# Performance work log

Measured on AMD Instinct MI355X. Metric: run time of the kernel, lower is better.

The kernel has to match this reference:

```python
import jax, jax.numpy as jnp
import numpy as np

B, S = 128, 32
V, E, H, L = 32000, 512, 1024, 2


def setup_inputs() -> dict:
    key = jax.random.key(0)
    ks = jax.random.split(key, 16)
    s = 0.02  # weight scale
    inp = {
        "x": jax.random.randint(ks[0], (B, S), 0, V),
        "encoder_output": jax.random.normal(ks[1], (S, B, H), jnp.float32),  # unused by module
        "encoder_hidden_state": jax.random.normal(ks[2], (L, B, H), jnp.float32),
        "emb": jax.random.normal(ks[3], (V, E), jnp.float32) * s,
        "w_ih0": jax.random.normal(ks[4], (3 * H, E), jnp.float32) * s,
        "w_hh0": jax.random.normal(ks[5], (3 * H, H), jnp.float32) * s,
        "b_ih0": jax.random.normal(ks[6], (3 * H,), jnp.float32) * s,
        "b_hh0": jax.random.normal(ks[7], (3 * H,), jnp.float32) * s,
        "w_ih1": jax.random.normal(ks[8], (3 * H, H), jnp.float32) * s,
        "w_hh1": jax.random.normal(ks[9], (3 * H, H), jnp.float32) * s,
        "b_ih1": jax.random.normal(ks[10], (3 * H,), jnp.float32) * s,
        "b_hh1": jax.random.normal(ks[11], (3 * H,), jnp.float32) * s,
        "w_dec": jax.random.normal(ks[12], (V, H), jnp.float32) * s,
        "b_dec": jax.random.normal(ks[13], (V,), jnp.float32) * s,
        "max_seq_length": S,
    }
    return inp


def _gru_cell(h, xt, w_ih, w_hh, b_ih, b_hh):
    # PyTorch GRU gate math
    gi = xt @ w_ih.T + b_ih  # [B, 3H]
    gh = h @ w_hh.T + b_hh   # [B, 3H]
    ir, iz, inn = jnp.split(gi, 3, axis=-1)
    hr, hz, hn = jnp.split(gh, 3, axis=-1)
    r = jax.nn.sigmoid(ir + hr)
    z = jax.nn.sigmoid(iz + hz)
    n = jnp.tanh(inn + r * hn)
    return (1.0 - z) * n + z * h


def reference(x, encoder_output, encoder_hidden_state, emb,
              w_ih0, w_hh0, b_ih0, b_hh0,
              w_ih1, w_hh1, b_ih1, b_hh1,
              w_dec, b_dec, max_seq_length):
    # teaching_rate = 0.0 -> pure teacher forcing; dropout p=0.0 -> identity.
    # Step 0 consumes SOS token (id 1, from torch.ones().long()); steps 1..T-1 consume x[:, i].
    Bsz = x.shape[0]
    sos = jnp.ones((Bsz, 1), jnp.int32)
    toks = jnp.concatenate([sos, x[:, 1:max_seq_length].astype(jnp.int32)], axis=1)  # [B, T]
    xs = emb[toks].transpose(1, 0, 2)  # [T, B, E] (seq-first, matching permute(1,0,2))

    def step(carry, xt):
        h0, h1 = carry
        h0 = _gru_cell(h0, xt, w_ih0, w_hh0, b_ih0, b_hh0)
        h1 = _gru_cell(h1, h0, w_ih1, w_hh1, b_ih1, b_hh1)
        return (h0, h1), h1

    init = (encoder_hidden_state[0], encoder_hidden_state[1])
    _, ys = jax.lax.scan(step, init, xs)  # ys: [T, B, H]
    logits = jnp.einsum('tbh,vh->tbv', ys, w_dec) + b_dec  # [T, B, V]
    return logits
```

## Files before the change

kernel.cpp:

```cpp
#include <hip/hip_runtime.h>
#include <hip/hip_bf16.h>
#include <stdint.h>

#define T_SEQ 32
#define BATCH 128
#define EMB   512
#define HID   1024
#define VOC   32000
#define G3    (3 * HID)
#define MROWS (T_SEQ * BATCH)
#define BHID  (BATCH * HID)

typedef __bf16 bf16_t;
typedef __bf16 bf16x8 __attribute__((ext_vector_type(8)));
typedef __bf16 bf16x4 __attribute__((ext_vector_type(4)));
typedef float  f32x4  __attribute__((ext_vector_type(4)));

#define MFMA(a, b, c) __builtin_amdgcn_mfma_f32_16x16x32_bf16((a), (b), (c), 0, 0, 0)

__global__ void f32_to_bf16_kernel(const float* __restrict__ in,
                                   bf16_t* __restrict__ out, int n) {
    int i = (blockIdx.x * blockDim.x + threadIdx.x) * 4;
    if (i + 3 < n) {
        float4 v = *(const float4*)(in + i);
        out[i + 0] = (bf16_t)v.x;
        out[i + 1] = (bf16_t)v.y;
        out[i + 2] = (bf16_t)v.z;
        out[i + 3] = (bf16_t)v.w;
    } else {
        for (; i < n; ++i) out[i] = (bf16_t)in[i];
    }
}

__global__ void embed_kernel(const int* __restrict__ x,
                             const float* __restrict__ emb,
                             bf16_t* __restrict__ X) {
    int m = blockIdx.x;
    int t = m >> 7, b = m & 127;
    int tok = (t == 0) ? 1 : x[b * T_SEQ + t];
    const float* src = emb + (size_t)tok * EMB;
    bf16_t* dst = X + (size_t)m * EMB;
    int c = threadIdx.x * 4;
    float4 v = *(const float4*)(src + c);
    dst[c + 0] = (bf16_t)v.x;
    dst[c + 1] = (bf16_t)v.y;
    dst[c + 2] = (bf16_t)v.z;
    dst[c + 3] = (bf16_t)v.w;
}

#define GLOAD_LDS16(g, l)                                                    \
    __builtin_amdgcn_global_load_lds(                                        \
        (const __attribute__((address_space(1))) void*)(g),                  \
        (__attribute__((address_space(3))) void*)(l), 16, 0, 0)

template <int BIAS>
__global__ __launch_bounds__(256) void gemm_bf16_kernel(
    const bf16_t* __restrict__ A, const bf16_t* __restrict__ B,
    const float* __restrict__ bias, float* __restrict__ C,
    int M, int N, int K) {
    __shared__ __align__(16) bf16_t As[128 * 32];
    __shared__ __align__(16) bf16_t Bs[128 * 32];

    const int nbm = gridDim.y, nbn = gridDim.x;
    const int nwg = nbm * nbn;
    int lin = blockIdx.y * nbn + blockIdx.x;
    if ((nwg & 7) == 0) {
        int xcd = lin & 7, idx = lin >> 3;
        lin = xcd * (nwg >> 3) + idx;
    }
    const int bm = (lin % nbm) * 128;
    const int bn = (lin / nbm) * 128;

    const int tid  = threadIdx.x;
    const int lane = tid & 63;
    const int w    = tid >> 6;
    const int wr   = w >> 1, wc = w & 1;

    f32x4 acc[4][4] = {};

    const int lrow = tid >> 2;
    const int lcol = (tid & 3) * 8;
    const bf16_t* ag = A + (size_t)(bm + lrow) * K + lcol;
    const bf16_t* bg = B + (size_t)(bn + lrow) * K + lcol;
    bf16_t* asl0 = As + lrow * 32 + lcol;
    bf16_t* asl1 = As + (lrow + 64) * 32 + lcol;
    bf16_t* bsl0 = Bs + lrow * 32 + lcol;
    bf16_t* bsl1 = Bs + (lrow + 64) * 32 + lcol;

    const int r16 = lane & 15;
    const int kh  = (lane >> 4) * 8;

    for (int k0 = 0; k0 < K; k0 += 32) {
        GLOAD_LDS16(ag + k0, asl0);
        GLOAD_LDS16(ag + (size_t)64 * K + k0, asl1);
        GLOAD_LDS16(bg + k0, bsl0);
        GLOAD_LDS16(bg + (size_t)64 * K + k0, bsl1);
        __syncthreads();

        bf16x8 af[4], bf[4];
#pragma unroll
        for (int mi = 0; mi < 4; ++mi)
            af[mi] = *(const bf16x8*)(As + (wr * 64 + mi * 16 + r16) * 32 + kh);
#pragma unroll
        for (int ni = 0; ni < 4; ++ni)
            bf[ni] = *(const bf16x8*)(Bs + (wc * 64 + ni * 16 + r16) * 32 + kh);
#pragma unroll
        for (int mi = 0; mi < 4; ++mi)
#pragma unroll
            for (int ni = 0; ni < 4; ++ni)
                acc[mi][ni] = MFMA(af[mi], bf[ni], acc[mi][ni]);
        __syncthreads();
    }

#pragma unroll
    for (int mi = 0; mi < 4; ++mi) {
        const int row0 = bm + wr * 64 + mi * 16 + (lane >> 4) * 4;
#pragma unroll
        for (int ni = 0; ni < 4; ++ni) {
            const int col = bn + wc * 64 + ni * 16 + r16;
            float bv = 0.f;
            if (BIAS) bv = bias[col];
#pragma unroll
            for (int r = 0; r < 4; ++r)
                C[(size_t)(row0 + r) * N + col] = acc[mi][ni][r] + bv;
        }
    }
}

template <int BIAS>
__global__ __launch_bounds__(512, 1) void gemm256_bf16_kernel(
    const bf16_t* __restrict__ A, const bf16_t* __restrict__ B,
    const float* __restrict__ bias, float* __restrict__ C,
    int M, int N, int K) {
    __shared__ __align__(16) bf16_t lds[2 * 2 * 16384];

    const int NT = K >> 6;
    const int nbm = gridDim.y, nbn = gridDim.x;
    const int nwg = nbm * nbn;
    int lin = blockIdx.y * nbn + blockIdx.x;
    {
        int q = nwg >> 3, r = nwg & 7, x = lin & 7, i = lin >> 3;
        lin = (x < r ? x * (q + 1) : r * (q + 1) + (x - r) * q) + i;
    }
    const int bm = (lin % nbm) * 256;
    const int bn = (lin / nbm) * 256;

    const int tid = threadIdx.x, lane = tid & 63;
    const int w = tid >> 6, wm = w >> 2, wn = w & 3;
    const int r16 = lane & 15, sl = lane >> 4, r7 = r16 & 7;

    const int srow  = tid >> 3;
    const int sslot = (tid & 7) ^ (srow & 7);
    const bf16_t* agS = A + (size_t)(bm + srow) * K + sslot * 8;
    const bf16_t* bgS = B + (size_t)(bn + srow) * K + sslot * 8;

    const int colk0 = ((0 + sl) ^ r7) * 8;
    const int colk1 = ((4 + sl) ^ r7) * 8;
    const int arow = (wm * 128 + r16) * 64;
    const int brow = (wn * 64 + r16) * 64;

    f32x4 acc[8][4] = {};
    bf16x8 af[4][2], bf[4][2];

#pragma unroll
    for (int l = 0; l < 4; ++l)
        GLOAD_LDS16(agS + (size_t)(l * 64) * K, lds + l * 4096 + tid * 8);
#pragma unroll
    for (int l = 0; l < 4; ++l)
        GLOAD_LDS16(bgS + (size_t)(l * 64) * K, lds + 16384 + l * 4096 + tid * 8);
#pragma unroll
    for (int l = 0; l < 4; ++l)
        GLOAD_LDS16(agS + (size_t)(l * 64) * K + 64,
                    lds + 32768 + l * 4096 + tid * 8);
#pragma unroll
    for (int l = 0; l < 4; ++l)
        GLOAD_LDS16(bgS + (size_t)(l * 64) * K + 64,
                    lds + 49152 + l * 4096 + tid * 8);
    asm volatile("s_waitcnt vmcnt(8)" ::: "memory");
    __builtin_amdgcn_sched_barrier(0);
    __builtin_amdgcn_s_barrier();

#pragma unroll 1
    for (int kt = 0; kt < NT; ++kt) {
        const int cur = kt & 1;
        const bf16_t* Ab = lds + cur * 32768;
        const bf16_t* Bb = Ab + 16384;
        bf16_t* Sb = lds + cur * 32768;
        const bool st = (kt + 2 < NT);
        const size_t kof = (size_t)(kt + 2) * 64;

#pragma unroll
        for (int fr = 0; fr < 4; ++fr) {
            af[fr][0] = *(const bf16x8*)(Ab + arow + fr * 1024 + colk0);
            af[fr][1] = *(const bf16x8*)(Ab + arow + fr * 1024 + colk1);
        }
#pragma unroll
        for (int nf = 0; nf < 2; ++nf) {
            bf[nf][0] = *(const bf16x8*)(Bb + brow + nf * 1024 + colk0);
            bf[nf][1] = *(const bf16x8*)(Bb + brow + nf * 1024 + colk1);
        }
        __builtin_amdgcn_sched_barrier(0);
        __builtin_amdgcn_s_barrier();
        asm volatile("s_waitcnt lgkmcnt(0)" ::: "memory");
        __builtin_amdgcn_sched_barrier(0);
        __builtin_amdgcn_s_setprio(1);
#pragma unroll
        for (int fr = 0; fr < 4; ++fr)
#pragma unroll
            for (int nf = 0; nf < 2; ++nf) {
                acc[fr][nf] = MFMA(af[fr][0], bf[nf][0], acc[fr][nf]);
                acc[fr][nf] = MFMA(af[fr][1], bf[nf][1], acc[fr][nf]);
            }
        __builtin_amdgcn_s_setprio(0);
        __builtin_amdgcn_sched_barrier(0);
        __builtin_amdgcn_s_barrier();

#pragma unroll
        for (int nf = 2; nf < 4; ++nf) {
            bf[nf][0] = *(const bf16x8*)(Bb + brow + nf * 1024 + colk0);
            bf[nf][1] = *(const bf16x8*)(Bb + brow + nf * 1024 + colk1);
        }
        __builtin_amdgcn_sched_barrier(0);
        if (st) {
            GLOAD_LDS16(agS + kof, Sb + tid * 8);
            GLOAD_LDS16(agS + (size_t)128 * K + kof, Sb + 8192 + tid * 8);
        }
        __builtin_amdgcn_s_barrier();
        asm volatile("s_waitcnt lgkmcnt(0)" ::: "memory");
        __builtin_amdgcn_sched_barrier(0);
        __builtin_amdgcn_s_setprio(1);
#pragma unroll
        for (int fr = 0; fr < 4; ++fr)
#pragma unroll
            for (int nf = 2; nf < 4; ++nf) {
                acc[fr][nf] = MFMA(af[fr][0], bf[nf][0], acc[fr][nf]);
                acc[fr][nf] = MFMA(af[fr][1], bf[nf][1], acc[fr][nf]);
            }
        __builtin_amdgcn_s_setprio(0);
        __builtin_amdgcn_sched_barrier(0);
        __builtin_amdgcn_s_barrier();

#pragma unroll
        for (int fr = 0; fr < 4; ++fr) {
            af[fr][0] = *(const bf16x8*)(Ab + arow + (fr + 4) * 1024 + colk0);
            af[fr][1] = *(const bf16x8*)(Ab + arow + (fr + 4) * 1024 + colk1);
        }
        __builtin_amdgcn_sched_barrier(0);
        if (st) {
#pragma unroll
            for (int l = 0; l < 4; ++l)
                GLOAD_LDS16(bgS + (size_t)(l * 64) * K + kof,
                            Sb + 16384 + l * 4096 + tid * 8);
        }
        __builtin_amdgcn_s_barrier();
        asm volatile("s_waitcnt lgkmcnt(0)" ::: "memory");
        __builtin_amdgcn_sched_barrier(0);
        __builtin_amdgcn_s_setprio(1);
#pragma unroll
        for (int fr = 0; fr < 4; ++fr)
#pragma unroll
            for (int nf = 0; nf < 2; ++nf) {
                acc[fr + 4][nf] = MFMA(af[fr][0], bf[nf][0], acc[fr + 4][nf]);
                acc[fr + 4][nf] = MFMA(af[fr][1], bf[nf][1], acc[fr + 4][nf]);
            }
        __builtin_amdgcn_s_setprio(0);
        __builtin_amdgcn_sched_barrier(0);
        __builtin_amdgcn_s_barrier();

        if (st) {
            GLOAD_LDS16(agS + (size_t)64 * K + kof, Sb + 4096 + tid * 8);
            GLOAD_LDS16(agS + (size_t)192 * K + kof, Sb + 12288 + tid * 8);
        }
        if (kt + 2 < NT) {
            asm volatile("s_waitcnt vmcnt(8)" ::: "memory");
        } else if (kt + 1 < NT) {
            asm volatile("s_waitcnt vmcnt(0)" ::: "memory");
        }
        __builtin_amdgcn_sched_barrier(0);
        __builtin_amdgcn_s_setprio(1);
#pragma unroll
        for (int fr = 0; fr < 4; ++fr)
#pragma unroll
            for (int nf = 2; nf < 4; ++nf) {
                acc[fr + 4][nf] = MFMA(af[fr][0], bf[nf][0], acc[fr + 4][nf]);
                acc[fr + 4][nf] = MFMA(af[fr][1], bf[nf][1], acc[fr + 4][nf]);
            }
        __builtin_amdgcn_s_setprio(0);
        __builtin_amdgcn_sched_barrier(0);
        __builtin_amdgcn_s_barrier();
    }

#pragma unroll
    for (int fr = 0; fr < 8; ++fr) {
        const int row0 = bm + wm * 128 + fr * 16 + sl * 4;
#pragma unroll
        for (int nf = 0; nf < 4; ++nf) {
            const int col = bn + wn * 64 + nf * 16 + r16;
            float bv = 0.f;
            if (BIAS) bv = bias[col];
#pragma unroll
            for (int r = 0; r < 4; ++r)
                C[(size_t)(row0 + r) * N + col] = acc[fr][nf][r] + bv;
        }
    }
}

union U64cast  { bf16x4 v; unsigned long long u; };
union U128cast { f32x4 v; unsigned long long u[2]; };

__global__ __launch_bounds__(256, 1) void fused_scan_kernel(
    const bf16_t* __restrict__ h0ib, const bf16_t* __restrict__ h1ib,
    const float* __restrict__ enc_hid,
    const bf16_t* __restrict__ whh0, const bf16_t* __restrict__ wih1,
    const bf16_t* __restrict__ whh1,
    const float* __restrict__ bhh0, const float* __restrict__ bih1,
    const float* __restrict__ bhh1,
    float* __restrict__ Gi, bf16_t* __restrict__ H0b,
    bf16_t* __restrict__ H1b, unsigned* __restrict__ flags) {
    __shared__ __align__(16) float Sg[4][3][128][16];

    const int tid  = threadIdx.x;
    const int lane = tid & 63;
    const int w    = tid >> 6;
    const int role = blockIdx.x >> 6;
    const int cb   = blockIdx.x & 63;
    const int c0   = cb * 16;
    const int r16  = lane & 15;
    const int kq   = (lane >> 4) * 8;

    const bf16_t* whh = role == 0 ? whh0 : (role == 1 ? wih1 : whh1);
    const float*  bia = role == 0 ? bhh0 : (role == 1 ? bih1 : bhh1);

    bf16x8 wf[3][8];
#pragma unroll
    for (int g = 0; g < 3; ++g)
#pragma unroll
        for (int kf = 0; kf < 8; ++kf)
            wf[g][kf] = *(const bf16x8*)(
                whh + (size_t)(g * HID + c0 + r16) * HID + w * 256 + kf * 32 + kq);

    const int cg   = tid & 3;
    const int rloc = tid >> 2;
    const int ce   = c0 + cg * 4;

    float bh[3][4];
#pragma unroll
    for (int g = 0; g < 3; ++g)
#pragma unroll
        for (int j = 0; j < 4; ++j) bh[g][j] = bia[g * HID + ce + j];

    float hp[2][4];
    if (role != 1) {
        const float* h0f = enc_hid + (role == 2 ? BHID : 0);
#pragma unroll
        for (int i = 0; i < 2; ++i)
#pragma unroll
            for (int j = 0; j < 4; ++j)
                hp[i][j] = h0f[(size_t)(rloc + i * 64) * HID + ce + j];
    }

    for (int t = 0; t < T_SEQ; ++t) {
        if (role == 0) {
            if (t && tid < 64)
                while (__hip_atomic_load(&flags[tid], __ATOMIC_RELAXED,
                                         __HIP_MEMORY_SCOPE_SYSTEM) <
                       (unsigned)t)
                    __builtin_amdgcn_s_sleep(1);
        } else if (role == 1) {
            if (tid < 64)
                while (__hip_atomic_load(&flags[tid], __ATOMIC_RELAXED,
                                         __HIP_MEMORY_SCOPE_SYSTEM) <
                       (unsigned)(t + 1))
                    __builtin_amdgcn_s_sleep(1);
        } else {
            if (tid < 64) {
                while (__hip_atomic_load(&flags[64 + tid], __ATOMIC_RELAXED,
                                         __HIP_MEMORY_SCOPE_SYSTEM) <
                       (unsigned)(t + 1))
                    __builtin_amdgcn_s_sleep(1);
            } else if (tid < 128 && t) {
                while (__hip_atomic_load(&flags[128 + tid - 64],
                                         __ATOMIC_RELAXED,
                                         __HIP_MEMORY_SCOPE_SYSTEM) <
                       (unsigned)t)
                    __builtin_amdgcn_s_sleep(1);
            }
        }
        __syncthreads();

        f32x4 gi[2][3];
        if (role == 0) {
#pragma unroll
            for (int i = 0; i < 2; ++i) {
                const size_t gb =
                    ((size_t)t * BATCH + rloc + i * 64) * G3 + ce;
                gi[i][0] = *(const f32x4*)(Gi + gb);
                gi[i][1] = *(const f32x4*)(Gi + gb + HID);
                gi[i][2] = *(const f32x4*)(Gi + gb + 2 * HID);
            }
        } else if (role == 2) {
#pragma unroll
            for (int i = 0; i < 2; ++i) {
                const size_t gb =
                    ((size_t)t * BATCH + rloc + i * 64) * G3 + ce;
#pragma unroll
                for (int g = 0; g < 3; ++g) {
                    U128cast u;
                    const unsigned long long* p =
                        (const unsigned long long*)(Gi + gb + g * HID);
                    u.u[0] = __hip_atomic_load(p, __ATOMIC_RELAXED,
                                               __HIP_MEMORY_SCOPE_SYSTEM);
                    u.u[1] = __hip_atomic_load(p + 1, __ATOMIC_RELAXED,
                                               __HIP_MEMORY_SCOPE_SYSTEM);
                    gi[i][g] = u.v;
                }
            }
        }

        const bf16_t* hb =
            role == 0 ? (t ? H0b + (size_t)(t - 1) * BHID : h0ib)
          : role == 1 ? (H0b + (size_t)t * BHID)
                      : (t ? H1b + (size_t)(t - 1) * BHID : h1ib);

        f32x4 acc[3][8] = {};
        bf16x8 af[4][8];
#define LD_GROUP(buf, kf)                                                    \
    {                                                                        \
        const int kbase = w * 256 + (kf) * 32 + kq;                          \
        _Pragma("unroll") for (int rf = 0; rf < 8; ++rf)                     \
            af[buf][rf] =                                                    \
                *(const bf16x8*)(hb + (size_t)(rf * 16 + r16) * HID + kbase); \
    }
        LD_GROUP(0, 0)
        LD_GROUP(1, 1)
        LD_GROUP(2, 2)
#pragma unroll
        for (int kf = 0; kf < 8; ++kf) {
            if (kf + 3 < 8) LD_GROUP((kf + 3) & 3, kf + 3)
#pragma unroll
            for (int rf = 0; rf < 8; ++rf) {
                acc[0][rf] = MFMA(af[kf & 3][rf], wf[0][kf], acc[0][rf]);
                acc[1][rf] = MFMA(af[kf & 3][rf], wf[1][kf], acc[1][rf]);
                acc[2][rf] = MFMA(af[kf & 3][rf], wf[2][kf], acc[2][rf]);
            }
        }
#undef LD_GROUP

#pragma unroll
        for (int g = 0; g < 3; ++g)
#pragma unroll
            for (int rf = 0; rf < 8; ++rf)
#pragma unroll
                for (int r = 0; r < 4; ++r)
                    Sg[w][g][rf * 16 + (lane >> 4) * 4 + r][r16] = acc[g][rf][r];
        __syncthreads();

#pragma unroll
        for (int i = 0; i < 2; ++i) {
            const int row = rloc + i * 64;
            f32x4 gr = *(const f32x4*)&Sg[0][0][row][cg * 4];
            f32x4 gz = *(const f32x4*)&Sg[0][1][row][cg * 4];
            f32x4 gn = *(const f32x4*)&Sg[0][2][row][cg * 4];
#pragma unroll
            for (int ks = 1; ks < 4; ++ks) {
                gr += *(const f32x4*)&Sg[ks][0][row][cg * 4];
                gz += *(const f32x4*)&Sg[ks][1][row][cg * 4];
                gn += *(const f32x4*)&Sg[ks][2][row][cg * 4];
            }
            if (role == 1) {
                const size_t gb =
                    ((size_t)t * BATCH + row) * G3 + ce;
                U128cast s0, s1, s2;
#pragma unroll
                for (int j = 0; j < 4; ++j) {
                    s0.v[j] = gr[j] + bh[0][j];
                    s1.v[j] = gz[j] + bh[1][j];
                    s2.v[j] = gn[j] + bh[2][j];
                }
                unsigned long long* p0 = (unsigned long long*)(Gi + gb);
                unsigned long long* p1 = (unsigned long long*)(Gi + gb + HID);
                unsigned long long* p2 = (unsigned long long*)(Gi + gb + 2 * HID);
                __hip_atomic_store(p0, s0.u[0], __ATOMIC_RELAXED, __HIP_MEMORY_SCOPE_SYSTEM);
                __hip_atomic_store(p0 + 1, s0.u[1], __ATOMIC_RELAXED, __HIP_MEMORY_SCOPE_SYSTEM);
                __hip_atomic_store(p1, s1.u[0], __ATOMIC_RELAXED, __HIP_MEMORY_SCOPE_SYSTEM);
                __hip_atomic_store(p1 + 1, s1.u[1], __ATOMIC_RELAXED, __HIP_MEMORY_SCOPE_SYSTEM);
                __hip_atomic_store(p2, s2.u[0], __ATOMIC_RELAXED, __HIP_MEMORY_SCOPE_SYSTEM);
                __hip_atomic_store(p2 + 1, s2.u[1], __ATOMIC_RELAXED, __HIP_MEMORY_SCOPE_SYSTEM);
            } else {
                U64cast hb4;
#pragma unroll
                for (int j = 0; j < 4; ++j) {
                    float rr = 1.f / (1.f + __expf(-(gi[i][0][j] + gr[j] + bh[0][j])));
                    float zz = 1.f / (1.f + __expf(-(gi[i][1][j] + gz[j] + bh[1][j])));
                    float nn = tanhf(gi[i][2][j] + rr * (gn[j] + bh[2][j]));
                    float h  = (1.f - zz) * nn + zz * hp[i][j];
                    hp[i][j] = h;
                    hb4.v[j] = (bf16_t)h;
                }
                bf16_t* dst = (role == 0 ? H0b : H1b) +
                              (size_t)t * BHID + (size_t)row * HID + ce;
                __hip_atomic_store((unsigned long long*)dst, hb4.u,
                                   __ATOMIC_RELAXED, __HIP_MEMORY_SCOPE_SYSTEM);
            }
        }

        __syncthreads();
        if (tid == 0)
            __hip_atomic_store(&flags[role * 64 + cb], (unsigned)(t + 1),
                               __ATOMIC_RELAXED, __HIP_MEMORY_SCOPE_SYSTEM);
    }
}

extern "C" void kernel_launch(void* const* d_in, const int* in_sizes, int n_in,
                              void* d_out, int out_size, void* d_ws, size_t ws_size,
                              hipStream_t stream) {
    const int*   x        = (const int*)d_in[0];
    const float* enc_hid  = (const float*)d_in[2];
    const float* emb      = (const float*)d_in[3];
    const float* w_ih0    = (const float*)d_in[4];
    const float* w_hh0    = (const float*)d_in[5];
    const float* b_ih0    = (const float*)d_in[6];
    const float* b_hh0    = (const float*)d_in[7];
    const float* w_ih1    = (const float*)d_in[8];
    const float* w_hh1    = (const float*)d_in[9];
    const float* b_ih1    = (const float*)d_in[10];
    const float* b_hh1    = (const float*)d_in[11];
    const float* w_dec    = (const float*)d_in[12];
    const float* b_dec    = (const float*)d_in[13];
    float* out = (float*)d_out;

    char* ws = (char*)d_ws;
    size_t off = 0;
    auto alloc = [&](size_t bytes) {
        void* p = ws + off;
        off += (bytes + 255) & ~(size_t)255;
        return p;
    };
    unsigned* flags  = (unsigned*)alloc(1024);
    bf16_t* Xb     = (bf16_t*)alloc((size_t)MROWS * EMB * 2);
    bf16_t* Wih0b  = (bf16_t*)alloc((size_t)G3 * EMB * 2);
    bf16_t* Whh0b  = (bf16_t*)alloc((size_t)G3 * HID * 2);
    bf16_t* Wih1b  = (bf16_t*)alloc((size_t)G3 * HID * 2);
    bf16_t* Whh1b  = (bf16_t*)alloc((size_t)G3 * HID * 2);
    bf16_t* Wdecb  = (bf16_t*)alloc((size_t)VOC * HID * 2);
    bf16_t* h0ib   = (bf16_t*)alloc((size_t)BATCH * HID * 2);
    bf16_t* h1ib   = (bf16_t*)alloc((size_t)BATCH * HID * 2);
    float*  Gi     = (float*)alloc((size_t)MROWS * G3 * 4);
    bf16_t* H0b    = (bf16_t*)alloc((size_t)MROWS * HID * 2);
    bf16_t* H1b    = (bf16_t*)alloc((size_t)MROWS * HID * 2);

    hipMemsetAsync(flags, 0, 1024, stream);

    auto cvt = [&](const float* src, bf16_t* dst, int n) {
        int blocks = (n + 1023) / 1024;
        f32_to_bf16_kernel<<<blocks, 256, 0, stream>>>(src, dst, n);
    };

    cvt(w_ih0, Wih0b, G3 * EMB);
    cvt(w_hh0, Whh0b, G3 * HID);
    cvt(w_ih1, Wih1b, G3 * HID);
    cvt(w_hh1, Whh1b, G3 * HID);
    cvt(w_dec, Wdecb, VOC * HID);
    cvt(enc_hid, h0ib, BATCH * HID);
    cvt(enc_hid + BATCH * HID, h1ib, BATCH * HID);

    embed_kernel<<<MROWS, 128, 0, stream>>>(x, emb, Xb);

    gemm_bf16_kernel<1><<<dim3(G3 / 128, MROWS / 128), 256, 0, stream>>>(
        Xb, Wih0b, b_ih0, Gi, MROWS, G3, EMB);

    fused_scan_kernel<<<192, 256, 0, stream>>>(
        h0ib, h1ib, enc_hid, Whh0b, Wih1b, Whh1b,
        b_hh0, b_ih1, b_hh1, Gi, H0b, H1b, flags);

    gemm256_bf16_kernel<1><<<dim3(VOC / 256, MROWS / 256), 512, 0, stream>>>(
        H1b, Wdecb, b_dec, out, MROWS, VOC, HID);
}
```

Before: 947.0 us.

## Fuse GRU scan and decoder GEMM into persistent mega-kernel with flag-gated tiles

The recurrent scan and the vocabulary projection GEMM now run in one persistent kernel. 192 blocks run the GRU scan while the other 64 blocks pull 256x256 decoder tiles from an atomic counter. Each tile waits only on the layer-1 flags for the timesteps it covers, so the projection can start on early timesteps while later steps are still being computed. This is meant to hide the sequential scan latency behind the large GEMM. The costs are heavier block shapes (512 threads with half idle in scan blocks), co-residency and deadlock risk, and the counter has to be reset between calls.

```diff
diff --git a/kernel.cpp b/kernel.cpp
--- a/kernel.cpp
+++ b/kernel.cpp
@@ -10,6 +10,7 @@
 #define G3    (3 * HID)
 #define MROWS (T_SEQ * BATCH)
 #define BHID  (BATCH * HID)
+#define NTILE 2000
 
 typedef __bf16 bf16_t;
 typedef __bf16 bf16x8 __attribute__((ext_vector_type(8)));
@@ -17,6 +18,16 @@
 typedef float  f32x4  __attribute__((ext_vector_type(4)));
 
 #define MFMA(a, b, c) __builtin_amdgcn_mfma_f32_16x16x32_bf16((a), (b), (c), 0, 0, 0)
+
+union U64cast  { bf16x4 v; unsigned long long u; };
+union U128cast { f32x4 v; unsigned long long u[2]; };
+
+__device__ __forceinline__ unsigned flag_ld(const unsigned* p) {
+    return __hip_atomic_load(p, __ATOMIC_RELAXED, __HIP_MEMORY_SCOPE_SYSTEM);
+}
+__device__ __forceinline__ void flag_st(unsigned* p, unsigned v) {
+    __hip_atomic_store(p, v, __ATOMIC_RELAXED, __HIP_MEMORY_SCOPE_SYSTEM);
+}
 
 __global__ void f32_to_bf16_kernel(const float* __restrict__ in,
                                    bf16_t* __restrict__ out, int n) {
@@ -127,188 +138,7 @@
     }
 }
 
-template <int BIAS>
-__global__ __launch_bounds__(512, 1) void gemm256_bf16_kernel(
-    const bf16_t* __restrict__ A, const bf16_t* __restrict__ B,
-    const float* __restrict__ bias, float* __restrict__ C,
-    int M, int N, int K) {
-    __shared__ __align__(16) bf16_t lds[2 * 2 * 16384];
-
-    const int NT = K >> 6;
-    const int nbm = gridDim.y, nbn = gridDim.x;
-    const int nwg = nbm * nbn;
-    int lin = blockIdx.y * nbn + blockIdx.x;
-    {
-        int q = nwg >> 3, r = nwg & 7, x = lin & 7, i = lin >> 3;
-        lin = (x < r ? x * (q + 1) : r * (q + 1) + (x - r) * q) + i;
-    }
-    const int bm = (lin % nbm) * 256;
-    const int bn = (lin / nbm) * 256;
-
-    const int tid = threadIdx.x, lane = tid & 63;
-    const int w = tid >> 6, wm = w >> 2, wn = w & 3;
-    const int r16 = lane & 15, sl = lane >> 4, r7 = r16 & 7;
-
-    const int srow  = tid >> 3;
-    const int sslot = (tid & 7) ^ (srow & 7);
-    const bf16_t* agS = A + (size_t)(bm + srow) * K + sslot * 8;
-    const bf16_t* bgS = B + (size_t)(bn + srow) * K + sslot * 8;
-
-    const int colk0 = ((0 + sl) ^ r7) * 8;
-    const int colk1 = ((4 + sl) ^ r7) * 8;
-    const int arow = (wm * 128 + r16) * 64;
-    const int brow = (wn * 64 + r16) * 64;
-
-    f32x4 acc[8][4] = {};
-    bf16x8 af[4][2], bf[4][2];
-
-#pragma unroll
-    for (int l = 0; l < 4; ++l)
-        GLOAD_LDS16(agS + (size_t)(l * 64) * K, lds + l * 4096 + tid * 8);
-#pragma unroll
-    for (int l = 0; l < 4; ++l)
-        GLOAD_LDS16(bgS + (size_t)(l * 64) * K, lds + 16384 + l * 4096 + tid * 8);
-#pragma unroll
-    for (int l = 0; l < 4; ++l)
-        GLOAD_LDS16(agS + (size_t)(l * 64) * K + 64,
-                    lds + 32768 + l * 4096 + tid * 8);
-#pragma unroll
-    for (int l = 0; l < 4; ++l)
-        GLOAD_LDS16(bgS + (size_t)(l * 64) * K + 64,
-                    lds + 49152 + l * 4096 + tid * 8);
-    asm volatile("s_waitcnt vmcnt(8)" ::: "memory");
-    __builtin_amdgcn_sched_barrier(0);
-    __builtin_amdgcn_s_barrier();
-
-#pragma unroll 1
-    for (int kt = 0; kt < NT; ++kt) {
-        const int cur = kt & 1;
-        const bf16_t* Ab = lds + cur * 32768;
-        const bf16_t* Bb = Ab + 16384;
-        bf16_t* Sb = lds + cur * 32768;
-        const bool st = (kt + 2 < NT);
-        const size_t kof = (size_t)(kt + 2) * 64;
-
-#pragma unroll
-        for (int fr = 0; fr < 4; ++fr) {
-            af[fr][0] = *(const bf16x8*)(Ab + arow + fr * 1024 + colk0);
-            af[fr][1] = *(const bf16x8*)(Ab + arow + fr * 1024 + colk1);
-        }
-#pragma unroll
-        for (int nf = 0; nf < 2; ++nf) {
-            bf[nf][0] = *(const bf16x8*)(Bb + brow + nf * 1024 + colk0);
-            bf[nf][1] = *(const bf16x8*)(Bb + brow + nf * 1024 + colk1);
-        }
-        __builtin_amdgcn_sched_barrier(0);
-        __builtin_amdgcn_s_barrier();
-        asm volatile("s_waitcnt lgkmcnt(0)" ::: "memory");
-        __builtin_amdgcn_sched_barrier(0);
-        __builtin_amdgcn_s_setprio(1);
-#pragma unroll
-        for (int fr = 0; fr < 4; ++fr)
-#pragma unroll
-            for (int nf = 0; nf < 2; ++nf) {
-                acc[fr][nf] = MFMA(af[fr][0], bf[nf][0], acc[fr][nf]);
-                acc[fr][nf] = MFMA(af[fr][1], bf[nf][1], acc[fr][nf]);
-            }
-        __builtin_amdgcn_s_setprio(0);
-        __builtin_amdgcn_sched_barrier(0);
-        __builtin_amdgcn_s_barrier();
-
-#pragma unroll
-        for (int nf = 2; nf < 4; ++nf) {
-            bf[nf][0] = *(const bf16x8*)(Bb + brow + nf * 1024 + colk0);
-            bf[nf][1] = *(const bf16x8*)(Bb + brow + nf * 1024 + colk1);
-        }
-        __builtin_amdgcn_sched_barrier(0);
-        if (st) {
-            GLOAD_LDS16(agS + kof, Sb + tid * 8);
-            GLOAD_LDS16(agS + (size_t)128 * K + kof, Sb + 8192 + tid * 8);
-        }
-        __builtin_amdgcn_s_barrier();
-        asm volatile("s_waitcnt lgkmcnt(0)" ::: "memory");
-        __builtin_amdgcn_sched_barrier(0);
-        __builtin_amdgcn_s_setprio(1);
-#pragma unroll
-        for (int fr = 0; fr < 4; ++fr)
-#pragma unroll
-            for (int nf = 2; nf < 4; ++nf) {
-                acc[fr][nf] = MFMA(af[fr][0], bf[nf][0], acc[fr][nf]);
-                acc[fr][nf] = MFMA(af[fr][1], bf[nf][1], acc[fr][nf]);
-            }
-        __builtin_amdgcn_s_setprio(0);
-        __builtin_amdgcn_sched_barrier(0);
-        __builtin_amdgcn_s_barrier();
-
-#pragma unroll
-        for (int fr = 0; fr < 4; ++fr) {
-            af[fr][0] = *(const bf16x8*)(Ab + arow + (fr + 4) * 1024 + colk0);
-            af[fr][1] = *(const bf16x8*)(Ab + arow + (fr + 4) * 1024 + colk1);
-        }
-        __builtin_amdgcn_sched_barrier(0);
-        if (st) {
-#pragma unroll
-            for (int l = 0; l < 4; ++l)
-                GLOAD_LDS16(bgS + (size_t)(l * 64) * K + kof,
-                            Sb + 16384 + l * 4096 + tid * 8);
-        }
-        __builtin_amdgcn_s_barrier();
-        asm volatile("s_waitcnt lgkmcnt(0)" ::: "memory");
-        __builtin_amdgcn_sched_barrier(0);
-        __builtin_amdgcn_s_setprio(1);
-#pragma unroll
-        for (int fr = 0; fr < 4; ++fr)
-#pragma unroll
-            for (int nf = 0; nf < 2; ++nf) {
-                acc[fr + 4][nf] = MFMA(af[fr][0], bf[nf][0], acc[fr + 4][nf]);
-                acc[fr + 4][nf] = MFMA(af[fr][1], bf[nf][1], acc[fr + 4][nf]);
-            }
-        __builtin_amdgcn_s_setprio(0);
-        __builtin_amdgcn_sched_barrier(0);
-        __builtin_amdgcn_s_barrier();
-
-        if (st) {
-            GLOAD_LDS16(agS + (size_t)64 * K + kof, Sb + 4096 + tid * 8);
-            GLOAD_LDS16(agS + (size_t)192 * K + kof, Sb + 12288 + tid * 8);
-        }
-        if (kt + 2 < NT) {
-            asm volatile("s_waitcnt vmcnt(8)" ::: "memory");
-        } else if (kt + 1 < NT) {
-            asm volatile("s_waitcnt vmcnt(0)" ::: "memory");
-        }
-        __builtin_amdgcn_sched_barrier(0);
-        __builtin_amdgcn_s_setprio(1);
-#pragma unroll
-        for (int fr = 0; fr < 4; ++fr)
-#pragma unroll
-            for (int nf = 2; nf < 4; ++nf) {
-                acc[fr + 4][nf] = MFMA(af[fr][0], bf[nf][0], acc[fr + 4][nf]);
-                acc[fr + 4][nf] = MFMA(af[fr][1], bf[nf][1], acc[fr + 4][nf]);
-            }
-        __builtin_amdgcn_s_setprio(0);
-        __builtin_amdgcn_sched_barrier(0);
-        __builtin_amdgcn_s_barrier();
-    }
-
-#pragma unroll
-    for (int fr = 0; fr < 8; ++fr) {
-        const int row0 = bm + wm * 128 + fr * 16 + sl * 4;
-#pragma unroll
-        for (int nf = 0; nf < 4; ++nf) {
-            const int col = bn + wn * 64 + nf * 16 + r16;
-            float bv = 0.f;
-            if (BIAS) bv = bias[col];
-#pragma unroll
-            for (int r = 0; r < 4; ++r)
-                C[(size_t)(row0 + r) * N + col] = acc[fr][nf][r] + bv;
-        }
-    }
-}
-
-union U64cast  { bf16x4 v; unsigned long long u; };
-union U128cast { f32x4 v; unsigned long long u[2]; };
-
-__global__ __launch_bounds__(256, 1) void fused_scan_kernel(
+__global__ __launch_bounds__(512, 2) void mega_kernel(
     const bf16_t* __restrict__ h0ib, const bf16_t* __restrict__ h1ib,
     const float* __restrict__ enc_hid,
     const bf16_t* __restrict__ whh0, const bf16_t* __restrict__ wih1,
@@ -316,114 +146,115 @@
     const float* __restrict__ bhh0, const float* __restrict__ bih1,
     const float* __restrict__ bhh1,
     float* __restrict__ Gi, bf16_t* __restrict__ H0b,
-    bf16_t* __restrict__ H1b, unsigned* __restrict__ flags) {
-    __shared__ __align__(16) float Sg[4][3][128][16];
-
-    const int tid  = threadIdx.x;
-    const int lane = tid & 63;
-    const int w    = tid >> 6;
-    const int role = blockIdx.x >> 6;
-    const int cb   = blockIdx.x & 63;
-    const int c0   = cb * 16;
-    const int r16  = lane & 15;
-    const int kq   = (lane >> 4) * 8;
-
-    const bf16_t* whh = role == 0 ? whh0 : (role == 1 ? wih1 : whh1);
-    const float*  bia = role == 0 ? bhh0 : (role == 1 ? bih1 : bhh1);
-
-    bf16x8 wf[3][8];
-#pragma unroll
-    for (int g = 0; g < 3; ++g)
-#pragma unroll
-        for (int kf = 0; kf < 8; ++kf)
-            wf[g][kf] = *(const bf16x8*)(
-                whh + (size_t)(g * HID + c0 + r16) * HID + w * 256 + kf * 32 + kq);
-
-    const int cg   = tid & 3;
-    const int rloc = tid >> 2;
-    const int ce   = c0 + cg * 4;
-
-    float bh[3][4];
-#pragma unroll
-    for (int g = 0; g < 3; ++g)
-#pragma unroll
-        for (int j = 0; j < 4; ++j) bh[g][j] = bia[g * HID + ce + j];
-
-    float hp[2][4];
-    if (role != 1) {
-        const float* h0f = enc_hid + (role == 2 ? BHID : 0);
-#pragma unroll
-        for (int i = 0; i < 2; ++i)
-#pragma unroll
-            for (int j = 0; j < 4; ++j)
-                hp[i][j] = h0f[(size_t)(rloc + i * 64) * HID + ce + j];
-    }
-
-    for (int t = 0; t < T_SEQ; ++t) {
-        if (role == 0) {
-            if (t && tid < 64)
-                while (__hip_atomic_load(&flags[tid], __ATOMIC_RELAXED,
-                                         __HIP_MEMORY_SCOPE_SYSTEM) <
-                       (unsigned)t)
-                    __builtin_amdgcn_s_sleep(1);
-        } else if (role == 1) {
-            if (tid < 64)
-                while (__hip_atomic_load(&flags[tid], __ATOMIC_RELAXED,
-                                         __HIP_MEMORY_SCOPE_SYSTEM) <
-                       (unsigned)(t + 1))
-                    __builtin_amdgcn_s_sleep(1);
-        } else {
-            if (tid < 64) {
-                while (__hip_atomic_load(&flags[64 + tid], __ATOMIC_RELAXED,
-                                         __HIP_MEMORY_SCOPE_SYSTEM) <
-                       (unsigned)(t + 1))
-                    __builtin_amdgcn_s_sleep(1);
-            } else if (tid < 128 && t) {
-                while (__hip_atomic_load(&flags[128 + tid - 64],
-                                         __ATOMIC_RELAXED,
-                                         __HIP_MEMORY_SCOPE_SYSTEM) <
-                       (unsigned)t)
-                    __builtin_amdgcn_s_sleep(1);
+    bf16_t* __restrict__ H1b,
+    const bf16_t* __restrict__ Wdecb, const float* __restrict__ bdec,
+    float* __restrict__ out, unsigned* __restrict__ flags) {
+    __shared__ __align__(16) char smem[131072];
+    __shared__ unsigned tileShared;
+    unsigned* ctr = flags + 192;
+
+    const int tid = threadIdx.x;
+    const int bid = blockIdx.x;
+
+    if (bid < 192) {
+        float (*Sg)[3][128][16] = (float (*)[3][128][16])smem;
+        const int role = bid >> 6;
+        const int cb   = bid & 63;
+        const int c0   = cb * 16;
+        const int lane = tid & 63;
+        const int w    = tid >> 6;
+        const int r16  = lane & 15;
+        const int kq   = (lane >> 4) * 8;
+        const bool act = tid < 256;
+
+        const int cg   = tid & 3;
+        const int rloc = tid >> 2;
+        const int ce   = c0 + cg * 4;
+
+        bf16x8 wf[3][8];
+        float bh[3][4], hp[2][4];
+
+        if (act) {
+            const bf16_t* whh = role == 0 ? whh0 : (role == 1 ? wih1 : whh1);
+            const float*  bia = role == 0 ? bhh0 : (role == 1 ? bih1 : bhh1);
+#pragma unroll
+            for (int g = 0; g < 3; ++g)
+#pragma unroll
+                for (int kf = 0; kf < 8; ++kf)
+                    wf[g][kf] = *(const bf16x8*)(
+                        whh + (size_t)(g * HID + c0 + r16) * HID + w * 256 +
+                        kf * 32 + kq);
+#pragma unroll
+            for (int g = 0; g < 3; ++g)
+#pragma unroll
+                for (int j = 0; j < 4; ++j) bh[g][j] = bia[g * HID + ce + j];
+            if (role != 1) {
+                const float* h0f = enc_hid + (role == 2 ? BHID : 0);
+#pragma unroll
+                for (int i = 0; i < 2; ++i)
+#pragma unroll
+                    for (int j = 0; j < 4; ++j)
+                        hp[i][j] = h0f[(size_t)(rloc + i * 64) * HID + ce + j];
             }
         }
-        __syncthreads();
-
-        f32x4 gi[2][3];
-        if (role == 0) {
-#pragma unroll
-            for (int i = 0; i < 2; ++i) {
-                const size_t gb =
-                    ((size_t)t * BATCH + rloc + i * 64) * G3 + ce;
-                gi[i][0] = *(const f32x4*)(Gi + gb);
-                gi[i][1] = *(const f32x4*)(Gi + gb + HID);
-                gi[i][2] = *(const f32x4*)(Gi + gb + 2 * HID);
-            }
-        } else if (role == 2) {
-#pragma unroll
-            for (int i = 0; i < 2; ++i) {
-                const size_t gb =
-                    ((size_t)t * BATCH + rloc + i * 64) * G3 + ce;
-#pragma unroll
-                for (int g = 0; g < 3; ++g) {
-                    U128cast u;
-                    const unsigned long long* p =
-                        (const unsigned long long*)(Gi + gb + g * HID);
-                    u.u[0] = __hip_atomic_load(p, __ATOMIC_RELAXED,
-                                               __HIP_MEMORY_SCOPE_SYSTEM);
-                    u.u[1] = __hip_atomic_load(p + 1, __ATOMIC_RELAXED,
-                                               __HIP_MEMORY_SCOPE_SYSTEM);
-                    gi[i][g] = u.v;
-                }
-            }
-        }
-
-        const bf16_t* hb =
-            role == 0 ? (t ? H0b + (size_t)(t - 1) * BHID : h0ib)
-          : role == 1 ? (H0b + (size_t)t * BHID)
-                      : (t ? H1b + (size_t)(t - 1) * BHID : h1ib);
-
-        f32x4 acc[3][8] = {};
-        bf16x8 af[4][8];
+
+        for (int t = 0; t < T_SEQ; ++t) {
+            if (role == 0) {
+                if (t && tid < 64)
+                    while (flag_ld(&flags[tid]) < (unsigned)t)
+                        __builtin_amdgcn_s_sleep(1);
+            } else if (role == 1) {
+                if (tid < 64)
+                    while (flag_ld(&flags[tid]) < (unsigned)(t + 1))
+                        __builtin_amdgcn_s_sleep(1);
+            } else {
+                if (tid < 64) {
+                    while (flag_ld(&flags[64 + tid]) < (unsigned)(t + 1))
+                        __builtin_amdgcn_s_sleep(1);
+                } else if (tid < 128 && t) {
+                    while (flag_ld(&flags[128 + tid - 64]) < (unsigned)t)
+                        __builtin_amdgcn_s_sleep(1);
+                }
+            }
+            __syncthreads();
+
+            f32x4 gi[2][3];
+            if (act) {
+                if (role == 0) {
+#pragma unroll
+                    for (int i = 0; i < 2; ++i) {
+                        const size_t gb =
+                            ((size_t)t * BATCH + rloc + i * 64) * G3 + ce;
+                        gi[i][0] = *(const f32x4*)(Gi + gb);
+                        gi[i][1] = *(const f32x4*)(Gi + gb + HID);
+                        gi[i][2] = *(const f32x4*)(Gi + gb + 2 * HID);
+                    }
+                } else if (role == 2) {
+#pragma unroll
+                    for (int i = 0; i < 2; ++i) {
+                        const size_t gb =
+                            ((size_t)t * BATCH + rloc + i * 64) * G3 + ce;
+#pragma unroll
+                        for (int g = 0; g < 3; ++g) {
+                            U128cast u;
+                            const unsigned long long* p =
+                                (const unsigned long long*)(Gi + gb + g * HID);
+                            u.u[0] = __hip_atomic_load(p, __ATOMIC_RELAXED,
+                                                       __HIP_MEMORY_SCOPE_SYSTEM);
+                            u.u[1] = __hip_atomic_load(p + 1, __ATOMIC_RELAXED,
+                                                       __HIP_MEMORY_SCOPE_SYSTEM);
+                            gi[i][g] = u.v;
+                        }
+                    }
+                }
+
+                const bf16_t* hb =
+                    role == 0 ? (t ? H0b + (size_t)(t - 1) * BHID : h0ib)
+                  : role == 1 ? (H0b + (size_t)t * BHID)
+                              : (t ? H1b + (size_t)(t - 1) * BHID : h1ib);
+
+                f32x4 acc[3][8] = {};
+                bf16x8 af[4][8];
 #define LD_GROUP(buf, kf)                                                    \
     {                                                                        \
         const int kbase = w * 256 + (kf) * 32 + kq;                          \
@@ -431,83 +262,269 @@
             af[buf][rf] =                                                    \
                 *(const bf16x8*)(hb + (size_t)(rf * 16 + r16) * HID + kbase); \
     }
-        LD_GROUP(0, 0)
-        LD_GROUP(1, 1)
-        LD_GROUP(2, 2)
-#pragma unroll
-        for (int kf = 0; kf < 8; ++kf) {
-            if (kf + 3 < 8) LD_GROUP((kf + 3) & 3, kf + 3)
-#pragma unroll
-            for (int rf = 0; rf < 8; ++rf) {
-                acc[0][rf] = MFMA(af[kf & 3][rf], wf[0][kf], acc[0][rf]);
-                acc[1][rf] = MFMA(af[kf & 3][rf], wf[1][kf], acc[1][rf]);
-                acc[2][rf] = MFMA(af[kf & 3][rf], wf[2][kf], acc[2][rf]);
-            }
+                LD_GROUP(0, 0)
+                LD_GROUP(1, 1)
+                LD_GROUP(2, 2)
+#pragma unroll
+                for (int kf = 0; kf < 8; ++kf) {
+                    if (kf + 3 < 8) LD_GROUP((kf + 3) & 3, kf + 3)
+#pragma unroll
+                    for (int rf = 0; rf < 8; ++rf) {
+                        acc[0][rf] = MFMA(af[kf & 3][rf], wf[0][kf], acc[0][rf]);
+                        acc[1][rf] = MFMA(af[kf & 3][rf], wf[1][kf], acc[1][rf]);
+                        acc[2][rf] = MFMA(af[kf & 3][rf], wf[2][kf], acc[2][rf]);
+                    }
+                }
+#undef LD_GROUP
+
+#pragma unroll
+                for (int g = 0; g < 3; ++g)
+#pragma unroll
+                    for (int rf = 0; rf < 8; ++rf)
+#pragma unroll
+                        for (int r = 0; r < 4; ++r)
+                            Sg[w][g][rf * 16 + (lane >> 4) * 4 + r][r16] =
+                                acc[g][rf][r];
+            }
+            __syncthreads();
+
+            if (act) {
+#pragma unroll
+                for (int i = 0; i < 2; ++i) {
+                    const int row = rloc + i * 64;
+                    f32x4 gr = *(const f32x4*)&Sg[0][0][row][cg * 4];
+                    f32x4 gz = *(const f32x4*)&Sg[0][1][row][cg * 4];
+                    f32x4 gn = *(const f32x4*)&Sg[0][2][row][cg * 4];
+#pragma unroll
+                    for (int ks = 1; ks < 4; ++ks) {
+                        gr += *(const f32x4*)&Sg[ks][0][row][cg * 4];
+                        gz += *(const f32x4*)&Sg[ks][1][row][cg * 4];
+                        gn += *(const f32x4*)&Sg[ks][2][row][cg * 4];
+                    }
+                    if (role == 1) {
+                        const size_t gb = ((size_t)t * BATCH + row) * G3 + ce;
+                        U128cast s0, s1, s2;
+#pragma unroll
+                        for (int j = 0; j < 4; ++j) {
+                            s0.v[j] = gr[j] + bh[0][j];
+                            s1.v[j] = gz[j] + bh[1][j];
+                            s2.v[j] = gn[j] + bh[2][j];
+                        }
+                        unsigned long long* p0 = (unsigned long long*)(Gi + gb);
+                        unsigned long long* p1 = (unsigned long long*)(Gi + gb + HID);
+                        unsigned long long* p2 = (unsigned long long*)(Gi + gb + 2 * HID);
+                        __hip_atomic_store(p0, s0.u[0], __ATOMIC_RELAXED, __HIP_MEMORY_SCOPE_SYSTEM);
+                        __hip_atomic_store(p0 + 1, s0.u[1], __ATOMIC_RELAXED, __HIP_MEMORY_SCOPE_SYSTEM);
+                        __hip_atomic_store(p1, s1.u[0], __ATOMIC_RELAXED, __HIP_MEMORY_SCOPE_SYSTEM);
+                        __hip_atomic_store(p1 + 1, s1.u[1], __ATOMIC_RELAXED, __HIP_MEMORY_SCOPE_SYSTEM);
+                        __hip_atomic_store(p2, s2.u[0], __ATOMIC_RELAXED, __HIP_MEMORY_SCOPE_SYSTEM);
+                        __hip_atomic_store(p2 + 1, s2.u[1], __ATOMIC_RELAXED, __HIP_MEMORY_SCOPE_SYSTEM);
+                    } else {
+                        U64cast hb4;
+#pragma unroll
+                        for (int j = 0; j < 4; ++j) {
+                            float rr = 1.f / (1.f + __expf(-(gi[i][0][j] + gr[j] + bh[0][j])));
+                            float zz = 1.f / (1.f + __expf(-(gi[i][1][j] + gz[j] + bh[1][j])));
+                            float nn = tanhf(gi[i][2][j] + rr * (gn[j] + bh[2][j]));
+                            float h  = (1.f - zz) * nn + zz * hp[i][j];
+                            hp[i][j] = h;
+                            hb4.v[j] = (bf16_t)h;
+                        }
+                        bf16_t* dst = (role == 0 ? H0b : H1b) +
+                                      (size_t)t * BHID + (size_t)row * HID + ce;
+                        __hip_atomic_store((unsigned long long*)dst, hb4.u,
+                                           __ATOMIC_RELAXED,
+                                           __HIP_MEMORY_SCOPE_SYSTEM);
+                    }
+                }
+            }
+            __syncthreads();
+            if (tid == 0) flag_st(&flags[role * 64 + cb], (unsigned)(t + 1));
         }
-#undef LD_GROUP
-
-#pragma unroll
-        for (int g = 0; g < 3; ++g)
-#pragma unroll
-            for (int rf = 0; rf < 8; ++rf)
-#pragma unroll
-                for (int r = 0; r < 4; ++r)
-                    Sg[w][g][rf * 16 + (lane >> 4) * 4 + r][r16] = acc[g][rf][r];
-        __syncthreads();
-
-#pragma unroll
-        for (int i = 0; i < 2; ++i) {
-            const int row = rloc + i * 64;
-            f32x4 gr = *(const f32x4*)&Sg[0][0][row][cg * 4];
-            f32x4 gz = *(const f32x4*)&Sg[0][1][row][cg * 4];
-            f32x4 gn = *(const f32x4*)&Sg[0][2][row][cg * 4];
-#pragma unroll
-            for (int ks = 1; ks < 4; ++ks) {
-                gr += *(const f32x4*)&Sg[ks][0][row][cg * 4];
-                gz += *(const f32x4*)&Sg[ks][1][row][cg * 4];
-                gn += *(const f32x4*)&Sg[ks][2][row][cg * 4];
-            }
-            if (role == 1) {
-                const size_t gb =
-                    ((size_t)t * BATCH + row) * G3 + ce;
-                U128cast s0, s1, s2;
-#pragma unroll
-                for (int j = 0; j < 4; ++j) {
-                    s0.v[j] = gr[j] + bh[0][j];
-                    s1.v[j] = gz[j] + bh[1][j];
-                    s2.v[j] = gn[j] + bh[2][j];
-                }
-                unsigned long long* p0 = (unsigned long long*)(Gi + gb);
-                unsigned long long* p1 = (unsigned long long*)(Gi + gb + HID);
-                unsigned long long* p2 = (unsigned long long*)(Gi + gb + 2 * HID);
-                __hip_atomic_store(p0, s0.u[0], __ATOMIC_RELAXED, __HIP_MEMORY_SCOPE_SYSTEM);
-                __hip_atomic_store(p0 + 1, s0.u[1], __ATOMIC_RELAXED, __HIP_MEMORY_SCOPE_SYSTEM);
-                __hip_atomic_store(p1, s1.u[0], __ATOMIC_RELAXED, __HIP_MEMORY_SCOPE_SYSTEM);
-                __hip_atomic_store(p1 + 1, s1.u[1], __ATOMIC_RELAXED, __HIP_MEMORY_SCOPE_SYSTEM);
-                __hip_atomic_store(p2, s2.u[0], __ATOMIC_RELAXED, __HIP_MEMORY_SCOPE_SYSTEM);
-                __hip_atomic_store(p2 + 1, s2.u[1], __ATOMIC_RELAXED, __HIP_MEMORY_SCOPE_SYSTEM);
-            } else {
-                U64cast hb4;
-#pragma unroll
-                for (int j = 0; j < 4; ++j) {
-                    float rr = 1.f / (1.f + __expf(-(gi[i][0][j] + gr[j] + bh[0][j])));
-                    float zz = 1.f / (1.f + __expf(-(gi[i][1][j] + gz[j] + bh[1][j])));
-                    float nn = tanhf(gi[i][2][j] + rr * (gn[j] + bh[2][j]));
-                    float h  = (1.f - zz) * nn + zz * hp[i][j];
-                    hp[i][j] = h;
-                    hb4.v[j] = (bf16_t)h;
-                }
-                bf16_t* dst = (role == 0 ? H0b : H1b) +
-                              (size_t)t * BHID + (size_t)row * HID + ce;
-                __hip_atomic_store((unsigned long long*)dst, hb4.u,
-                                   __ATOMIC_RELAXED, __HIP_MEMORY_SCOPE_SYSTEM);
+    }
+
+    {
+        bf16_t* lds = (bf16_t*)smem;
+        const int K = HID;
+        const int lane = tid & 63;
+        const int w8 = tid >> 6, wm = w8 >> 2, wn = w8 & 3;
+        const int r16 = lane & 15, sl = lane >> 4, r7 = r16 & 7;
+        const int srow  = tid >> 3;
+        const int sslot = (tid & 7) ^ (srow & 7);
+        const int colk0 = ((0 + sl) ^ r7) * 8;
+        const int colk1 = ((4 + sl) ^ r7) * 8;
+        const int arow = (wm * 128 + r16) * 64;
+        const int brow = (wn * 64 + r16) * 64;
+
+        int have = 0;
+        for (;;) {
+            __syncthreads();
+            if (tid == 0)
+                tileShared = __hip_atomic_fetch_add(ctr, 1u, __ATOMIC_RELAXED,
+                                                    __HIP_MEMORY_SCOPE_AGENT);
+            __syncthreads();
+            const int tile = (int)tileShared;
+            if (tile >= NTILE) break;
+
+            const int rr_ = tile / 125, cc_ = tile - rr_ * 125;
+            const int bm = rr_ * 256, bn = cc_ * 256;
+            const int need = 2 * rr_ + 2;
+            if (need > have) {
+                if (tid < 64)
+                    while (flag_ld(&flags[128 + tid]) < (unsigned)need)
+                        __builtin_amdgcn_s_sleep(1);
+                __syncthreads();
+                have = need;
+            }
+
+            const bf16_t* agS = H1b + (size_t)(bm + srow) * K + sslot * 8;
+            const bf16_t* bgS = Wdecb + (size_t)(bn + srow) * K + sslot * 8;
+
+            f32x4 acc[8][4] = {};
+            bf16x8 af[4][2], bf[4][2];
+
+#pragma unroll
+            for (int l = 0; l < 4; ++l)
+                GLOAD_LDS16(agS + (size_t)(l * 64) * K, lds + l * 4096 + tid * 8);
+#pragma unroll
+            for (int l = 0; l < 4; ++l)
+                GLOAD_LDS16(bgS + (size_t)(l * 64) * K,
+                            lds + 16384 + l * 4096 + tid * 8);
+#pragma unroll
+            for (int l = 0; l < 4; ++l)
+                GLOAD_LDS16(agS + (size_t)(l * 64) * K + 64,
+                            lds + 32768 + l * 4096 + tid * 8);
+#pragma unroll
+            for (int l = 0; l < 4; ++l)
+                GLOAD_LDS16(bgS + (size_t)(l * 64) * K + 64,
+                            lds + 49152 + l * 4096 + tid * 8);
+            asm volatile("s_waitcnt vmcnt(8)" ::: "memory");
+            __builtin_amdgcn_sched_barrier(0);
+            __builtin_amdgcn_s_barrier();
+
+#pragma unroll 1
+            for (int kt = 0; kt < 16; ++kt) {
+                const int cur = kt & 1;
+                const bf16_t* Ab = lds + cur * 32768;
+                const bf16_t* Bb = Ab + 16384;
+                bf16_t* Sb = lds + cur * 32768;
+                const bool st = (kt + 2 < 16);
+                const size_t kof = (size_t)(kt + 2) * 64;
+
+#pragma unroll
+                for (int fr = 0; fr < 4; ++fr) {
+                    af[fr][0] = *(const bf16x8*)(Ab + arow + fr * 1024 + colk0);
+                    af[fr][1] = *(const bf16x8*)(Ab + arow + fr * 1024 + colk1);
+                }
+#pragma unroll
+                for (int nf = 0; nf < 2; ++nf) {
+                    bf[nf][0] = *(const bf16x8*)(Bb + brow + nf * 1024 + colk0);
+                    bf[nf][1] = *(const bf16x8*)(Bb + brow + nf * 1024 + colk1);
+                }
+                __builtin_amdgcn_sched_barrier(0);
+                __builtin_amdgcn_s_barrier();
+                asm volatile("s_waitcnt lgkmcnt(0)" ::: "memory");
+                __builtin_amdgcn_sched_barrier(0);
+                __builtin_amdgcn_s_setprio(1);
+#pragma unroll
+                for (int fr = 0; fr < 4; ++fr)
+#pragma unroll
+                    for (int nf = 0; nf < 2; ++nf) {
+                        acc[fr][nf] = MFMA(af[fr][0], bf[nf][0], acc[fr][nf]);
+                        acc[fr][nf] = MFMA(af[fr][1], bf[nf][1], acc[fr][nf]);
+                    }
+                __builtin_amdgcn_s_setprio(0);
+                __builtin_amdgcn_sched_barrier(0);
+                __builtin_amdgcn_s_barrier();
+
+#pragma unroll
+                for (int nf = 2; nf < 4; ++nf) {
+                    bf[nf][0] = *(const bf16x8*)(Bb + brow + nf * 1024 + colk0);
+                    bf[nf][1] = *(const bf16x8*)(Bb + brow + nf * 1024 + colk1);
+                }
+                __builtin_amdgcn_sched_barrier(0);
+                if (st) {
+                    GLOAD_LDS16(agS + kof, Sb + tid * 8);
+                    GLOAD_LDS16(agS + (size_t)128 * K + kof, Sb + 8192 + tid * 8);
+                }
+                __builtin_amdgcn_s_barrier();
+                asm volatile("s_waitcnt lgkmcnt(0)" ::: "memory");
+                __builtin_amdgcn_sched_barrier(0);
+                __builtin_amdgcn_s_setprio(1);
+#pragma unroll
+                for (int fr = 0; fr < 4; ++fr)
+#pragma unroll
+                    for (int nf = 2; nf < 4; ++nf) {
+                        acc[fr][nf] = MFMA(af[fr][0], bf[nf][0], acc[fr][nf]);
+                        acc[fr][nf] = MFMA(af[fr][1], bf[nf][1], acc[fr][nf]);
+                    }
+                __builtin_amdgcn_s_setprio(0);
+                __builtin_amdgcn_sched_barrier(0);
+                __builtin_amdgcn_s_barrier();
+
+#pragma unroll
+                for (int fr = 0; fr < 4; ++fr) {
+                    af[fr][0] = *(const bf16x8*)(Ab + arow + (fr + 4) * 1024 + colk0);
+                    af[fr][1] = *(const bf16x8*)(Ab + arow + (fr + 4) * 1024 + colk1);
+                }
+                __builtin_amdgcn_sched_barrier(0);
+                if (st) {
+#pragma unroll
+                    for (int l = 0; l < 4; ++l)
+                        GLOAD_LDS16(bgS + (size_t)(l * 64) * K + kof,
+                                    Sb + 16384 + l * 4096 + tid * 8);
+                }
+                __builtin_amdgcn_s_barrier();
+                asm volatile("s_waitcnt lgkmcnt(0)" ::: "memory");
+                __builtin_amdgcn_sched_barrier(0);
+                __builtin_amdgcn_s_setprio(1);
+#pragma unroll
+                for (int fr = 0; fr < 4; ++fr)
+#pragma unroll
+                    for (int nf = 0; nf < 2; ++nf) {
+                        acc[fr + 4][nf] = MFMA(af[fr][0], bf[nf][0], acc[fr + 4][nf]);
+                        acc[fr + 4][nf] = MFMA(af[fr][1], bf[nf][1], acc[fr + 4][nf]);
+                    }
+                __builtin_amdgcn_s_setprio(0);
+                __builtin_amdgcn_sched_barrier(0);
+                __builtin_amdgcn_s_barrier();
+
+                if (st) {
+                    GLOAD_LDS16(agS + (size_t)64 * K + kof, Sb + 4096 + tid * 8);
+                    GLOAD_LDS16(agS + (size_t)192 * K + kof, Sb + 12288 + tid * 8);
+                }
+                if (kt + 2 < 16) {
+                    asm volatile("s_waitcnt vmcnt(8)" ::: "memory");
+                } else if (kt + 1 < 16) {
+                    asm volatile("s_waitcnt vmcnt(0)" ::: "memory");
+                }
+                __builtin_amdgcn_sched_barrier(0);
+                __builtin_amdgcn_s_setprio(1);
+#pragma unroll
+                for (int fr = 0; fr < 4; ++fr)
+#pragma unroll
+                    for (int nf = 2; nf < 4; ++nf) {
+                        acc[fr + 4][nf] = MFMA(af[fr][0], bf[nf][0], acc[fr + 4][nf]);
+                        acc[fr + 4][nf] = MFMA(af[fr][1], bf[nf][1], acc[fr + 4][nf]);
+                    }
+                __builtin_amdgcn_s_setprio(0);
+                __builtin_amdgcn_sched_barrier(0);
+                __builtin_amdgcn_s_barrier();
+            }
+
+#pragma unroll
+            for (int fr = 0; fr < 8; ++fr) {
+                const int row0 = bm + wm * 128 + fr * 16 + sl * 4;
+#pragma unroll
+                for (int nf = 0; nf < 4; ++nf) {
+                    const int col = bn + wn * 64 + nf * 16 + r16;
+                    const float bv = bdec[col];
+#pragma unroll
+                    for (int r = 0; r < 4; ++r)
+                        out[(size_t)(row0 + r) * VOC + col] = acc[fr][nf][r] + bv;
+                }
             }
         }
-
-        __syncthreads();
-        if (tid == 0)
-            __hip_atomic_store(&flags[role * 64 + cb], (unsigned)(t + 1),
-                               __ATOMIC_RELAXED, __HIP_MEMORY_SCOPE_SYSTEM);
     }
 }
 
@@ -569,10 +586,8 @@
     gemm_bf16_kernel<1><<<dim3(G3 / 128, MROWS / 128), 256, 0, stream>>>(
         Xb, Wih0b, b_ih0, Gi, MROWS, G3, EMB);
 
-    fused_scan_kernel<<<192, 256, 0, stream>>>(
+    mega_kernel<<<256, 512, 0, stream>>>(
         h0ib, h1ib, enc_hid, Whh0b, Wih1b, Whh1b,
-        b_hh0, b_ih1, b_hh1, Gi, H0b, H1b, flags);
-
-    gemm256_bf16_kernel<1><<<dim3(VOC / 256, MROWS / 256), 512, 0, stream>>>(
-        H1b, Wdecb, b_dec, out, MROWS, VOC, HID);
-}
+        b_hh0, b_ih1, b_hh1, Gi, H0b, H1b,
+        Wdecb, b_dec, out, flags);
+}
```

Measured after the change: 1.020 ms. 1.08x slower.
